# Kernel tuning notes

Measured on AMD Instinct MI355X. Metric: run time of the kernel, lower is better.

## Reference

```python
import jax, jax.numpy as jnp
import numpy as np

C = 256      # channels
G = 8        # groups
K = 9        # 3x3 sampling points (DCNv4 default kernel_size=3)
DWK = 3      # dw_kernel_size (wrapper passes kernel_size=3)
OFFSET_SCALE = 1.0
N, H, W = 8, 64, 64


def setup_inputs() -> dict:
    key = jax.random.key(0)
    ks = jax.random.split(key, 6)
    def init(k, shape, fan):
        return jax.random.normal(k, shape, jnp.float32) * (fan ** -0.5)
    return {
        "x": jax.random.normal(ks[0], (N, C, H, W), jnp.float32),
        "dw_w": init(ks[1], (C, 1, DWK, DWK), DWK * DWK),   # depthwise conv (OIHW, groups=C)
        "dw_b": jnp.zeros((C,), jnp.float32),
        "om_w": init(ks[2], (G * K * 3, C), C) * 0.01,       # offset/mask linear (small offsets)
        "om_b": jnp.zeros((G * K * 3,), jnp.float32),
        "vp_w": init(ks[3], (C, C), C),                      # value_proj
        "vp_b": jnp.zeros((C,), jnp.float32),
        "op_w": init(ks[4], (C, C), C),                      # output_proj (output_bias=False)
    }


def reference(x, dw_w, dw_b, om_w, om_b, vp_w, vp_b, op_w):
    n, c, h, w = x.shape
    cg = c // G
    L = h * w
    # b c h w -> b (h w) c
    xf = x.transpose(0, 2, 3, 1).reshape(n, L, c)
    value = (xf @ vp_w.T + vp_b).reshape(n, L, G, cg)
    # offset/mask branch: depthwise conv on raw input, then linear
    om_in = jax.lax.conv_general_dilated(
        x, dw_w, (1, 1), "SAME", feature_group_count=c,
        dimension_numbers=("NCHW", "OIHW", "NCHW")) + dw_b[None, :, None, None]
    om = om_in.transpose(0, 2, 3, 1).reshape(n, L, c) @ om_w.T + om_b  # (n, L, G*K*3)
    om = om.reshape(n, h, w, G, K * 3)
    off = om[..., : 2 * K].reshape(n, h, w, G, K, 2) * OFFSET_SCALE     # (dy, dx) per point
    mask = om[..., 2 * K:]                                              # (n,h,w,G,K) raw (DCNv4: no softmax)
    # base 3x3 dilation-1 grid centered at each pixel
    d = jnp.arange(-1, 2, dtype=jnp.float32)
    dy, dx = jnp.meshgrid(d, d, indexing="ij")
    base = jnp.stack([dy.ravel(), dx.ravel()], -1)  # (K, 2)
    py = (jnp.arange(h, dtype=jnp.float32).reshape(1, h, 1, 1, 1)
          + base[:, 0].reshape(1, 1, 1, 1, K) + off[..., 0])  # (n,h,w,G,K)
    px = (jnp.arange(w, dtype=jnp.float32).reshape(1, 1, w, 1, 1)
          + base[:, 1].reshape(1, 1, 1, 1, K) + off[..., 1])
    y0 = jnp.floor(py); x0 = jnp.floor(px)
    ty = py - y0; tx = px - x0
    y0i = y0.astype(jnp.int32); x0i = x0.astype(jnp.int32)

    def gather(yi, xi, wgt):
        valid = (yi >= 0) & (yi < h) & (xi >= 0) & (xi < w)
        idx = jnp.clip(yi, 0, h - 1) * w + jnp.clip(xi, 0, w - 1)       # (n,h,w,G,K)
        idx = idx.transpose(0, 1, 2, 4, 3).reshape(n, L * K, G)[..., None]
        g = jnp.take_along_axis(value, idx, axis=1)                     # (n, L*K, G, cg)
        g = g.reshape(n, h, w, K, G, cg).transpose(0, 1, 2, 4, 3, 5)    # (n,h,w,G,K,cg)
        return g * (wgt * valid)[..., None]

    sampled = (gather(y0i,     x0i,     (1 - ty) * (1 - tx))
             + gather(y0i,     x0i + 1, (1 - ty) * tx)
             + gather(y0i + 1, x0i,     ty * (1 - tx))
             + gather(y0i + 1, x0i + 1, ty * tx))
    out = jnp.einsum("nhwgk,nhwgkc->nhwgc", mask, sampled)  # mask-weighted aggregation
    out = out.reshape(n, L, c) @ op_w.T                      # output_proj (no bias)
    # b (h w) c -> b c h w
    return out.reshape(n, h, w, c).transpose(0, 3, 1, 2)
```

## Files before the change

kernel.cpp:

```cpp
#include <hip/hip_runtime.h>
#include <math.h>

#define N_  8
#define C_  256
#define G_  8
#define CG_ 32
#define K_  9
#define H_  64
#define W_  64
#define L_  (H_*W_)
#define OM_ 216
#define OMP_ 256

using frag_ab = __attribute__((ext_vector_type(8))) short;
using frag_cd = __attribute__((ext_vector_type(4))) float;

__device__ __forceinline__ unsigned short f2bf(float f) {
    unsigned int u = __float_as_uint(f);
    u += 0x7FFFu + ((u >> 16) & 1u);
    return (unsigned short)(u >> 16);
}
__device__ __forceinline__ float bflo(unsigned int u) { return __uint_as_float(u << 16); }
__device__ __forceinline__ float bfhi(unsigned int u) { return __uint_as_float(u & 0xFFFF0000u); }

__device__ __forceinline__ void gld16(const void* g, void* l) {
    __builtin_amdgcn_global_load_lds((const __attribute__((address_space(1))) void*)g,
                                     (__attribute__((address_space(3))) void*)l, 16, 0, 0);
}

__global__ __launch_bounds__(256) void cvt_weights(const float* __restrict__ vp_w,
                                                   const float* __restrict__ om_w,
                                                   const float* __restrict__ om_b,
                                                   const float* __restrict__ op_w,
                                                   unsigned short* __restrict__ vp_wb,
                                                   unsigned short* __restrict__ om_wb,
                                                   float* __restrict__ om_bp,
                                                   unsigned short* __restrict__ op_wb) {
    int idx = blockIdx.x * 256 + threadIdx.x;
    if (idx < C_ * C_) {
        vp_wb[idx] = f2bf(vp_w[idx]);
        op_wb[idx] = f2bf(op_w[idx]);
        om_wb[idx] = (idx < OM_ * C_) ? f2bf(om_w[idx]) : (unsigned short)0;
    }
    if (idx < OMP_) om_bp[idx] = (idx < OM_) ? om_b[idx] : 0.f;
}

__global__ __launch_bounds__(256) void prep_kernel(const float* __restrict__ x,
                                                   const float* __restrict__ w,
                                                   const float* __restrict__ b,
                                                   unsigned short* __restrict__ xb,
                                                   unsigned short* __restrict__ omb) {
    const int n = blockIdx.z, y = blockIdx.y, c0 = blockIdx.x * 32;
    const int tid = threadIdx.x;
    __shared__ float xs[3][32][66];
    __shared__ __align__(16) unsigned short os[2][64][40];
    if (tid < 192) {
        int r = tid / 64, c = (tid / 2) % 32, e = tid & 1;
        xs[r][c][e * 65] = 0.f;
    }
    const float* xbase = x + ((size_t)n * C_ + c0) * L_;
    for (int i = tid; i < 3 * 32 * 16; i += 256) {
        int r = i >> 9, rem = i & 511, c = rem >> 4, x4 = (rem & 15) * 4;
        int yy = y + r - 1;
        float4 v = make_float4(0.f, 0.f, 0.f, 0.f);
        if ((unsigned)yy < (unsigned)H_) v = *(const float4*)(xbase + (size_t)c * L_ + yy * W_ + x4);
        xs[r][c][1 + x4] = v.x; xs[r][c][2 + x4] = v.y;
        xs[r][c][3 + x4] = v.z; xs[r][c][4 + x4] = v.w;
    }
    __syncthreads();

    const int c = tid & 31, x0 = (tid >> 5) * 8;
    float wv[9];
#pragma unroll
    for (int i = 0; i < 9; i++) wv[i] = w[(c0 + c) * 9 + i];
    const float bias = b[c0 + c];
    float o[8];
#pragma unroll
    for (int j = 0; j < 8; j++) o[j] = bias;
#pragma unroll
    for (int r = 0; r < 3; r++) {
        float v[10];
#pragma unroll
        for (int d = 0; d < 10; d++) v[d] = xs[r][c][x0 + d];
#pragma unroll
        for (int j = 0; j < 8; j++)
            o[j] += wv[r * 3] * v[j] + wv[r * 3 + 1] * v[j + 1] + wv[r * 3 + 2] * v[j + 2];
    }
#pragma unroll
    for (int j = 0; j < 8; j++) {
        os[0][x0 + j][c] = f2bf(xs[1][c][1 + x0 + j]);
        os[1][x0 + j][c] = f2bf(o[j]);
    }
    __syncthreads();

    const int l = tid >> 2, c8 = (tid & 3) * 8;
    uint4 va = *(const uint4*)&os[0][l][c8];
    uint4 vc = *(const uint4*)&os[1][l][c8];
    size_t dst = ((size_t)n * L_ + y * W_ + l) * C_ + c0 + c8;
    *(uint4*)(xb + dst) = va;
    *(uint4*)(omb + dst) = vc;
}

template <bool BF16_OUT, bool BIAS>
__global__ __launch_bounds__(256) void gemm_bf16(const unsigned short* __restrict__ A,
                                                 const unsigned short* __restrict__ B,
                                                 const float* __restrict__ bias,
                                                 void* __restrict__ Dv,
                                                 int drow, long bbatch, long dbatch) {
    __shared__ unsigned short As[128 * 32];
    __shared__ unsigned short Bs[128 * 32];
    const int tid = threadIdx.x;
    const long i0 = (long)blockIdx.x * 128;
    const long j0 = (long)blockIdx.y * 128;
    const unsigned short* Ab = A + i0 * C_;
    const unsigned short* Bb = B + bbatch * blockIdx.z + j0 * C_;
    const int wave = tid >> 6, lane = tid & 63;
    const int iw = (wave & 1) * 64, jw = (wave >> 1) * 64;
    const int lm = lane & 15, kq = lane >> 4;
    const int srow = tid >> 2, scol = (tid & 3) * 8;

    frag_cd acc[4][4];
#pragma unroll
    for (int a = 0; a < 4; a++)
#pragma unroll
        for (int c = 0; c < 4; c++) acc[a][c] = (frag_cd){0.f, 0.f, 0.f, 0.f};

    for (int k0 = 0; k0 < C_; k0 += 32) {
        const unsigned short* ga0 = Ab + (long)srow * C_ + k0 + scol;
        const unsigned short* gb0 = Bb + (long)srow * C_ + k0 + scol;
        gld16(ga0,            As + tid * 8);
        gld16(ga0 + 64 * C_,  As + 2048 + tid * 8);
        gld16(gb0,            Bs + tid * 8);
        gld16(gb0 + 64 * C_,  Bs + 2048 + tid * 8);
        __syncthreads();
        frag_ab af[4], bfr[4];
#pragma unroll
        for (int mi = 0; mi < 4; mi++)
            af[mi] = *(const frag_ab*)&As[(iw + mi * 16 + lm) * 32 + kq * 8];
#pragma unroll
        for (int ni = 0; ni < 4; ni++)
            bfr[ni] = *(const frag_ab*)&Bs[(jw + ni * 16 + lm) * 32 + kq * 8];
#pragma unroll
        for (int mi = 0; mi < 4; mi++)
#pragma unroll
            for (int ni = 0; ni < 4; ni++)
                acc[mi][ni] = __builtin_amdgcn_mfma_f32_16x16x32_bf16(af[mi], bfr[ni], acc[mi][ni], 0, 0, 0);
        __syncthreads();
    }

    float bv[4];
#pragma unroll
    for (int ni = 0; ni < 4; ni++)
        bv[ni] = BIAS ? bias[(int)(j0 + jw + ni * 16 + lm)] : 0.f;

    const long ibase = i0 + iw + kq * 4;
    const long jbase = j0 + jw + lm;
    const long dz = dbatch * blockIdx.z;
#pragma unroll
    for (int mi = 0; mi < 4; mi++) {
#pragma unroll
        for (int ni = 0; ni < 4; ni++) {
            long j = jbase + ni * 16;
#pragma unroll
            for (int r = 0; r < 4; r++) {
                long i = ibase + mi * 16 + r;
                float v = acc[mi][ni][r] + bv[ni];
                if (BF16_OUT)
                    ((unsigned short*)Dv)[dz + i * drow + j] = f2bf(v);
                else
                    ((float*)Dv)[dz + i * drow + j] = v;
            }
        }
    }
}

__global__ __launch_bounds__(256) void sample_kernel(const unsigned short* __restrict__ value,
                                                     const float* __restrict__ om,
                                                     unsigned short* __restrict__ interm) {
    const int n = blockIdx.y;
    const int l0 = blockIdx.x * 8;
    const int tid = threadIdx.x;

    __shared__ float sOm[8 * OM_];
    __shared__ float4 wgt[64][9];
    __shared__ uint4  soff[64][9];

    const float* omsrc = om + ((size_t)n * L_ + l0) * OMP_;
    for (int i = tid; i < 8 * OM_; i += 256) {
        int pp = i / OM_;
        sOm[i] = omsrc[pp * OMP_ + (i - pp * OM_)];
    }
    __syncthreads();

    for (int it = tid; it < 576; it += 256) {
        int pair = it / 9, k = it - pair * 9;
        int p = pair >> 3, g = pair & 7;
        int l = l0 + p, y = l >> 6, xp2 = l & 63;
        const float* so = &sOm[p * OM_ + g * 27];
        float offy = so[2 * k], offx = so[2 * k + 1], mk = so[18 + k];
        float py = (float)(y + k / 3 - 1) + offy;
        float px = (float)(xp2 + k % 3 - 1) + offx;
        float fy = floorf(py), fx = floorf(px);
        float ty = py - fy, tx = px - fx;
        int y0 = (int)fy, x0i = (int)fx;
        int y1 = y0 + 1, x1 = x0i + 1;
        float vy0 = ((unsigned)y0 < (unsigned)H_) ? 1.f : 0.f;
        float vy1 = ((unsigned)y1 < (unsigned)H_) ? 1.f : 0.f;
        float vx0 = ((unsigned)x0i < (unsigned)W_) ? 1.f : 0.f;
        float vx1 = ((unsigned)x1 < (unsigned)W_) ? 1.f : 0.f;
        int cy0 = min(max(y0, 0), H_ - 1), cy1 = min(max(y1, 0), H_ - 1);
        int cx0 = min(max(x0i, 0), W_ - 1), cx1 = min(max(x1, 0), W_ - 1);
        wgt[pair][k] = make_float4(mk * (1.f - ty) * (1.f - tx) * vy0 * vx0,
                                   mk * (1.f - ty) * tx         * vy0 * vx1,
                                   mk * ty         * (1.f - tx) * vy1 * vx0,
                                   mk * ty         * tx         * vy1 * vx1);
        soff[pair][k] = make_uint4((unsigned)((cy0 * W_ + cx0) << 9),
                                   (unsigned)((cy0 * W_ + cx1) << 9),
                                   (unsigned)((cy1 * W_ + cx0) << 9),
                                   (unsigned)((cy1 * W_ + cx1) << 9));
    }
    __syncthreads();

    const int pair = tid >> 2, p = pair >> 3, g = pair & 7, c8 = (tid & 3) * 8;
    const char* vb = (const char*)(value + (size_t)n * L_ * C_ + g * CG_ + c8);
    float acc[8] = {0.f, 0.f, 0.f, 0.f, 0.f, 0.f, 0.f, 0.f};
#pragma unroll
    for (int k = 0; k < K_; k++) {
        float4 wk = wgt[pair][k];
        uint4  ok = soff[pair][k];
        const uint4 v00 = *(const uint4*)(vb + ok.x);
        const uint4 v01 = *(const uint4*)(vb + ok.y);
        const uint4 v10 = *(const uint4*)(vb + ok.z);
        const uint4 v11 = *(const uint4*)(vb + ok.w);
#define ACC8(V, WW) { \
        acc[0] += WW * bflo(V.x); acc[1] += WW * bfhi(V.x); \
        acc[2] += WW * bflo(V.y); acc[3] += WW * bfhi(V.y); \
        acc[4] += WW * bflo(V.z); acc[5] += WW * bfhi(V.z); \
        acc[6] += WW * bflo(V.w); acc[7] += WW * bfhi(V.w); }
        ACC8(v00, wk.x) ACC8(v01, wk.y) ACC8(v10, wk.z) ACC8(v11, wk.w)
#undef ACC8
    }
    uint4 pk;
    unsigned short* pp2 = (unsigned short*)&pk;
#pragma unroll
    for (int i = 0; i < 8; i++) pp2[i] = f2bf(acc[i]);
    *(uint4*)(interm + ((size_t)n * L_ + l0 + p) * C_ + g * CG_ + c8) = pk;
}

extern "C" void kernel_launch(void* const* d_in, const int* in_sizes, int n_in,
                              void* d_out, int out_size, void* d_ws, size_t ws_size,
                              hipStream_t stream) {
    const float* x    = (const float*)d_in[0];
    const float* dw_w = (const float*)d_in[1];
    const float* dw_b = (const float*)d_in[2];
    const float* om_w = (const float*)d_in[3];
    const float* om_b = (const float*)d_in[4];
    const float* vp_w = (const float*)d_in[5];
    const float* vp_b = (const float*)d_in[6];
    const float* op_w = (const float*)d_in[7];
    float* out = (float*)d_out;

    char* ws = (char*)d_ws;
    unsigned short* xb      = (unsigned short*)(ws);
    unsigned short* omb     = (unsigned short*)(ws + 16777216);
    unsigned short* valueb  = (unsigned short*)(ws + 33554432);
    float*          omf     = (float*)(ws + 50331648);
    unsigned short* vp_wb   = (unsigned short*)(ws + 83886080);
    unsigned short* om_wb   = (unsigned short*)(ws + 84017152);
    unsigned short* op_wb   = (unsigned short*)(ws + 84148224);
    float*          om_bp   = (float*)(ws + 84279296);
    unsigned short* intermb = xb;

    cvt_weights<<<dim3(256), 256, 0, stream>>>(vp_w, om_w, om_b, op_w,
                                               vp_wb, om_wb, om_bp, op_wb);
    prep_kernel<<<dim3(C_ / 32, H_, N_), 256, 0, stream>>>(x, dw_w, dw_b, xb, omb);
    gemm_bf16<true, true><<<dim3(256, 2, 1), 256, 0, stream>>>(
        xb, vp_wb, vp_b, valueb, C_, 0, 0);
    gemm_bf16<false, true><<<dim3(256, 2, 1), 256, 0, stream>>>(
        omb, om_wb, om_bp, omf, OMP_, 0, 0);
    sample_kernel<<<dim3(L_ / 8, N_), 256, 0, stream>>>(valueb, omf, intermb);
    gemm_bf16<false, false><<<dim3(2, 32, N_), 256, 0, stream>>>(
        op_wb, intermb, nullptr, out, L_, (long)L_ * C_, (long)C_ * L_);
}
```

Measured before the change: 176.4 us.

## Fuse sampling with output projection and merge value/offset GEMMs into one launch

```diff
diff --git a/kernel.cpp b/kernel.cpp
--- a/kernel.cpp
+++ b/kernel.cpp
@@ -101,19 +101,25 @@
     *(uint4*)(omb + dst) = vc;
 }
 
-template <bool BF16_OUT, bool BIAS>
-__global__ __launch_bounds__(256) void gemm_bf16(const unsigned short* __restrict__ A,
-                                                 const unsigned short* __restrict__ B,
-                                                 const float* __restrict__ bias,
-                                                 void* __restrict__ Dv,
-                                                 int drow, long bbatch, long dbatch) {
+__global__ __launch_bounds__(256) void gemm12_kernel(const unsigned short* __restrict__ xb,
+                                                     const unsigned short* __restrict__ omb,
+                                                     const unsigned short* __restrict__ vp_wb,
+                                                     const unsigned short* __restrict__ om_wb,
+                                                     const float* __restrict__ vp_b,
+                                                     const float* __restrict__ om_bp,
+                                                     unsigned short* __restrict__ valueb,
+                                                     float* __restrict__ omf) {
     __shared__ unsigned short As[128 * 32];
     __shared__ unsigned short Bs[128 * 32];
+    const int which = blockIdx.z;
+    const unsigned short* A = which ? omb : xb;
+    const unsigned short* B = which ? om_wb : vp_wb;
+    const float* bias = which ? om_bp : vp_b;
     const int tid = threadIdx.x;
     const long i0 = (long)blockIdx.x * 128;
     const long j0 = (long)blockIdx.y * 128;
     const unsigned short* Ab = A + i0 * C_;
-    const unsigned short* Bb = B + bbatch * blockIdx.z + j0 * C_;
+    const unsigned short* Bb = B + j0 * C_;
     const int wave = tid >> 6, lane = tid & 63;
     const int iw = (wave & 1) * 64, jw = (wave >> 1) * 64;
     const int lm = lane & 15, kq = lane >> 4;
@@ -151,11 +157,10 @@
     float bv[4];
 #pragma unroll
     for (int ni = 0; ni < 4; ni++)
-        bv[ni] = BIAS ? bias[(int)(j0 + jw + ni * 16 + lm)] : 0.f;
+        bv[ni] = bias[(int)(j0 + jw + ni * 16 + lm)];
 
     const long ibase = i0 + iw + kq * 4;
     const long jbase = j0 + jw + lm;
-    const long dz = dbatch * blockIdx.z;
 #pragma unroll
     for (int mi = 0; mi < 4; mi++) {
 #pragma unroll
@@ -165,86 +170,122 @@
             for (int r = 0; r < 4; r++) {
                 long i = ibase + mi * 16 + r;
                 float v = acc[mi][ni][r] + bv[ni];
-                if (BF16_OUT)
-                    ((unsigned short*)Dv)[dz + i * drow + j] = f2bf(v);
+                if (which)
+                    omf[i * OMP_ + j] = v;
                 else
-                    ((float*)Dv)[dz + i * drow + j] = v;
+                    valueb[i * C_ + j] = f2bf(v);
             }
         }
     }
 }
 
-__global__ __launch_bounds__(256) void sample_kernel(const unsigned short* __restrict__ value,
-                                                     const float* __restrict__ om,
-                                                     unsigned short* __restrict__ interm) {
-    const int n = blockIdx.y;
-    const int l0 = blockIdx.x * 8;
+__global__ __launch_bounds__(256) void sampleout_kernel(const unsigned short* __restrict__ value,
+                                                        const float* __restrict__ om,
+                                                        const unsigned short* __restrict__ opw,
+                                                        float* __restrict__ out) {
+    const int n = blockIdx.y, l0 = blockIdx.x * 64;
     const int tid = threadIdx.x;
-
-    __shared__ float sOm[8 * OM_];
-    __shared__ float4 wgt[64][9];
-    __shared__ uint4  soff[64][9];
-
-    const float* omsrc = om + ((size_t)n * L_ + l0) * OMP_;
-    for (int i = tid; i < 8 * OM_; i += 256) {
-        int pp = i / OM_;
-        sOm[i] = omsrc[pp * OMP_ + (i - pp * OM_)];
+    __shared__ __align__(16) unsigned short interm[64 * 256];
+
+    const size_t vbase = (size_t)n * L_ * C_;
+#pragma unroll
+    for (int rep = 0; rep < 2; rep++) {
+        const int pair = tid + rep * 256;
+        const int p = pair >> 3, g = pair & 7;
+        const int l = l0 + p, y = l >> 6, xp = l & 63;
+        const float* so = om + ((size_t)n * L_ + l) * OMP_ + g * 27;
+        const char* vp = (const char*)(value + vbase + g * CG_);
+        float acc[32];
+#pragma unroll
+        for (int c = 0; c < 32; c++) acc[c] = 0.f;
+#pragma unroll
+        for (int k = 0; k < K_; k++) {
+            float offy = so[2 * k], offx = so[2 * k + 1], mk = so[18 + k];
+            float py = (float)(y + k / 3 - 1) + offy;
+            float px = (float)(xp + k % 3 - 1) + offx;
+            float fy = floorf(py), fx = floorf(px);
+            float ty = py - fy, tx = px - fx;
+            int y0 = (int)fy, x0i = (int)fx;
+            int y1 = y0 + 1, x1 = x0i + 1;
+            float vy0 = ((unsigned)y0 < (unsigned)H_) ? 1.f : 0.f;
+            float vy1 = ((unsigned)y1 < (unsigned)H_) ? 1.f : 0.f;
+            float vx0 = ((unsigned)x0i < (unsigned)W_) ? 1.f : 0.f;
+            float vx1 = ((unsigned)x1 < (unsigned)W_) ? 1.f : 0.f;
+            int cy0 = min(max(y0, 0), H_ - 1), cy1 = min(max(y1, 0), H_ - 1);
+            int cx0 = min(max(x0i, 0), W_ - 1), cx1 = min(max(x1, 0), W_ - 1);
+            float w00 = mk * (1.f - ty) * (1.f - tx) * vy0 * vx0;
+            float w01 = mk * (1.f - ty) * tx         * vy0 * vx1;
+            float w10 = mk * ty         * (1.f - tx) * vy1 * vx0;
+            float w11 = mk * ty         * tx         * vy1 * vx1;
+            unsigned o00 = (unsigned)((cy0 * W_ + cx0) * (C_ * 2));
+            unsigned o01 = (unsigned)((cy0 * W_ + cx1) * (C_ * 2));
+            unsigned o10 = (unsigned)((cy1 * W_ + cx0) * (C_ * 2));
+            unsigned o11 = (unsigned)((cy1 * W_ + cx1) * (C_ * 2));
+#define UNP8(U, BOF, WW) { \
+            acc[BOF+0] += WW * bflo(U.x); acc[BOF+1] += WW * bfhi(U.x); \
+            acc[BOF+2] += WW * bflo(U.y); acc[BOF+3] += WW * bfhi(U.y); \
+            acc[BOF+4] += WW * bflo(U.z); acc[BOF+5] += WW * bfhi(U.z); \
+            acc[BOF+6] += WW * bflo(U.w); acc[BOF+7] += WW * bfhi(U.w); }
+#define CORNER(OFF, WW) { \
+            const uint4* cp = (const uint4*)(vp + OFF); \
+            uint4 u0 = cp[0], u1 = cp[1], u2 = cp[2], u3 = cp[3]; \
+            UNP8(u0, 0, WW) UNP8(u1, 8, WW) UNP8(u2, 16, WW) UNP8(u3, 24, WW) }
+            CORNER(o00, w00) CORNER(o01, w01) CORNER(o10, w10) CORNER(o11, w11)
+#undef CORNER
+#undef UNP8
+        }
+#pragma unroll
+        for (int j = 0; j < 4; j++) {
+            uint4 pk;
+            unsigned short* ps = (unsigned short*)&pk;
+#pragma unroll
+            for (int e = 0; e < 8; e++) ps[e] = f2bf(acc[j * 8 + e]);
+            int phys = (g * 4 + j) ^ (p & 7);
+            *(uint4*)&interm[p * 256 + phys * 8] = pk;
+        }
     }
     __syncthreads();
 
-    for (int it = tid; it < 576; it += 256) {
-        int pair = it / 9, k = it - pair * 9;
-        int p = pair >> 3, g = pair & 7;
-        int l = l0 + p, y = l >> 6, xp2 = l & 63;
-        const float* so = &sOm[p * OM_ + g * 27];
-        float offy = so[2 * k], offx = so[2 * k + 1], mk = so[18 + k];
-        float py = (float)(y + k / 3 - 1) + offy;
-        float px = (float)(xp2 + k % 3 - 1) + offx;
-        float fy = floorf(py), fx = floorf(px);
-        float ty = py - fy, tx = px - fx;
-        int y0 = (int)fy, x0i = (int)fx;
-        int y1 = y0 + 1, x1 = x0i + 1;
-        float vy0 = ((unsigned)y0 < (unsigned)H_) ? 1.f : 0.f;
-        float vy1 = ((unsigned)y1 < (unsigned)H_) ? 1.f : 0.f;
-        float vx0 = ((unsigned)x0i < (unsigned)W_) ? 1.f : 0.f;
-        float vx1 = ((unsigned)x1 < (unsigned)W_) ? 1.f : 0.f;
-        int cy0 = min(max(y0, 0), H_ - 1), cy1 = min(max(y1, 0), H_ - 1);
-        int cx0 = min(max(x0i, 0), W_ - 1), cx1 = min(max(x1, 0), W_ - 1);
-        wgt[pair][k] = make_float4(mk * (1.f - ty) * (1.f - tx) * vy0 * vx0,
-                                   mk * (1.f - ty) * tx         * vy0 * vx1,
-                                   mk * ty         * (1.f - tx) * vy1 * vx0,
-                                   mk * ty         * tx         * vy1 * vx1);
-        soff[pair][k] = make_uint4((unsigned)((cy0 * W_ + cx0) << 9),
-                                   (unsigned)((cy0 * W_ + cx1) << 9),
-                                   (unsigned)((cy1 * W_ + cx0) << 9),
-                                   (unsigned)((cy1 * W_ + cx1) << 9));
-    }
-    __syncthreads();
-
-    const int pair = tid >> 2, p = pair >> 3, g = pair & 7, c8 = (tid & 3) * 8;
-    const char* vb = (const char*)(value + (size_t)n * L_ * C_ + g * CG_ + c8);
-    float acc[8] = {0.f, 0.f, 0.f, 0.f, 0.f, 0.f, 0.f, 0.f};
-#pragma unroll
-    for (int k = 0; k < K_; k++) {
-        float4 wk = wgt[pair][k];
-        uint4  ok = soff[pair][k];
-        const uint4 v00 = *(const uint4*)(vb + ok.x);
-        const uint4 v01 = *(const uint4*)(vb + ok.y);
-        const uint4 v10 = *(const uint4*)(vb + ok.z);
-        const uint4 v11 = *(const uint4*)(vb + ok.w);
-#define ACC8(V, WW) { \
-        acc[0] += WW * bflo(V.x); acc[1] += WW * bfhi(V.x); \
-        acc[2] += WW * bflo(V.y); acc[3] += WW * bfhi(V.y); \
-        acc[4] += WW * bflo(V.z); acc[5] += WW * bfhi(V.z); \
-        acc[6] += WW * bflo(V.w); acc[7] += WW * bfhi(V.w); }
-        ACC8(v00, wk.x) ACC8(v01, wk.y) ACC8(v10, wk.z) ACC8(v11, wk.w)
-#undef ACC8
-    }
-    uint4 pk;
-    unsigned short* pp2 = (unsigned short*)&pk;
-#pragma unroll
-    for (int i = 0; i < 8; i++) pp2[i] = f2bf(acc[i]);
-    *(uint4*)(interm + ((size_t)n * L_ + l0 + p) * C_ + g * CG_ + c8) = pk;
+    const int wave = tid >> 6, lane = tid & 63;
+    const int lm = lane & 15, kq = lane >> 4;
+    const int q0w = wave * 64;
+    frag_cd acc2[4][4];
+#pragma unroll
+    for (int a = 0; a < 4; a++)
+#pragma unroll
+        for (int c = 0; c < 4; c++) acc2[a][c] = (frag_cd){0.f, 0.f, 0.f, 0.f};
+
+    for (int k0 = 0; k0 < C_; k0 += 32) {
+        frag_ab af[4], bfr[4];
+#pragma unroll
+        for (int mi = 0; mi < 4; mi++)
+            af[mi] = *(const frag_ab*)(opw + (size_t)(q0w + mi * 16 + lm) * C_ + k0 + kq * 8);
+#pragma unroll
+        for (int ni = 0; ni < 4; ni++) {
+            int pxr = ni * 16 + lm;
+            int phys = (k0 / 8 + kq) ^ (pxr & 7);
+            bfr[ni] = *(const frag_ab*)&interm[pxr * 256 + phys * 8];
+        }
+#pragma unroll
+        for (int mi = 0; mi < 4; mi++)
+#pragma unroll
+            for (int ni = 0; ni < 4; ni++)
+                acc2[mi][ni] = __builtin_amdgcn_mfma_f32_16x16x32_bf16(af[mi], bfr[ni], acc2[mi][ni], 0, 0, 0);
+    }
+
+    float* ob = out + (size_t)n * C_ * L_ + l0;
+#pragma unroll
+    for (int mi = 0; mi < 4; mi++) {
+#pragma unroll
+        for (int ni = 0; ni < 4; ni++) {
+            int pxr = ni * 16 + lm;
+#pragma unroll
+            for (int r = 0; r < 4; r++) {
+                int q = q0w + mi * 16 + kq * 4 + r;
+                ob[(size_t)q * L_ + pxr] = acc2[mi][ni][r];
+            }
+        }
+    }
 }
 
 extern "C" void kernel_launch(void* const* d_in, const int* in_sizes, int n_in,
@@ -269,16 +310,11 @@
     unsigned short* om_wb   = (unsigned short*)(ws + 84017152);
     unsigned short* op_wb   = (unsigned short*)(ws + 84148224);
     float*          om_bp   = (float*)(ws + 84279296);
-    unsigned short* intermb = xb;
 
     cvt_weights<<<dim3(256), 256, 0, stream>>>(vp_w, om_w, om_b, op_w,
                                                vp_wb, om_wb, om_bp, op_wb);
     prep_kernel<<<dim3(C_ / 32, H_, N_), 256, 0, stream>>>(x, dw_w, dw_b, xb, omb);
-    gemm_bf16<true, true><<<dim3(256, 2, 1), 256, 0, stream>>>(
-        xb, vp_wb, vp_b, valueb, C_, 0, 0);
-    gemm_bf16<false, true><<<dim3(256, 2, 1), 256, 0, stream>>>(
-        omb, om_wb, om_bp, omf, OMP_, 0, 0);
-    sample_kernel<<<dim3(L_ / 8, N_), 256, 0, stream>>>(valueb, omf, intermb);
-    gemm_bf16<false, false><<<dim3(2, 32, N_), 256, 0, stream>>>(
-        op_wb, intermb, nullptr, out, L_, (long)L_ * C_, (long)C_ * L_);
-}
+    gemm12_kernel<<<dim3(256, 2, 2), 256, 0, stream>>>(
+        xb, omb, vp_wb, om_wb, vp_b, om_bp, valueb, omf);
+    sampleout_kernel<<<dim3(L_ / 64, N_), 256, 0, stream>>>(valueb, omf, op_wb, out);
+}
```

Measured after the change: 201.9 us. +14.4%, slower.
